# Kernel tuning notes

Hardware: AMD Instinct MI355X
Metric: run time of the kernel (lower is better)

Reference implementation:

```python
import jax, jax.numpy as jnp
import numpy as np

NQ = 6          # num_qubits
BS = 3          # basis_size (Pauli x,y,z)
HID = 32        # LSTM hidden size
SNAPS = 16      # max_num_snapshots
BATCH = 1024
DIM = 2 ** NQ   # 64


def _pauli():
    sx = np.array([[0., 1.], [1., 0.]], dtype=np.complex64)
    sy = np.array([[0., -1j], [1j, 0.]], dtype=np.complex64)
    sz = np.array([[1., 0.], [0., -1.]], dtype=np.complex64)
    return np.stack([sx, sy, sz], axis=0)


def setup_inputs():
    key = jax.random.key(0)
    ks = jax.random.split(key, 12)
    snapshot = jax.random.uniform(ks[0], (BATCH, NQ), jnp.float32, -1.0, 1.0)
    basis_comp_vector = jax.nn.softmax(
        jax.random.normal(ks[1], (BATCH, NQ, BS), jnp.float32), axis=-1)
    # valid density matrices: rho = A A^dag / tr
    ar = jax.random.normal(ks[2], (BATCH, DIM, DIM), jnp.float32)
    ai = jax.random.normal(ks[3], (BATCH, DIM, DIM), jnp.float32)
    A = ar + 1j * ai
    rho_c = jnp.einsum('bij,bkj->bik', A, jnp.conj(A))
    tr = jnp.trace(rho_c, axis1=1, axis2=2)[:, None, None]
    rho_c = rho_c / tr
    rho = jnp.stack([jnp.real(rho_c), jnp.imag(rho_c)], axis=1).astype(jnp.float32)
    h0 = jax.random.normal(ks[4], (BATCH, HID), jnp.float32)
    c0 = jax.random.normal(ks[5], (BATCH, HID), jnp.float32)
    in_dim = NQ + NQ * BS
    W_ih = jax.random.normal(ks[6], (4 * HID, in_dim), jnp.float32) * 0.1
    W_hh = jax.random.normal(ks[7], (4 * HID, HID), jnp.float32) * 0.1
    b_ih = jax.random.normal(ks[8], (4 * HID,), jnp.float32) * 0.05
    b_hh = jax.random.normal(ks[9], (4 * HID,), jnp.float32) * 0.05
    Wp = jax.random.normal(ks[10], (NQ, HID, BS), jnp.float32) * 0.1
    bp = jax.random.normal(ks[11], (NQ, BS), jnp.float32) * 0.05
    pauli = _pauli()
    basis_r = jnp.asarray(np.real(pauli), jnp.float32)
    basis_i = jnp.asarray(np.imag(pauli), jnp.float32)
    return {"snapshot": snapshot, "basis_comp_vector": basis_comp_vector,
            "rho": rho, "h0": h0, "c0": c0,
            "W_ih": W_ih, "W_hh": W_hh, "b_ih": b_ih, "b_hh": b_hh,
            "Wp": Wp, "bp": bp, "basis_r": basis_r, "basis_i": basis_i}


def _apply(p, M, axis, b):
    # apply 2x2 batched operator M [b,2,2] on tensor axis `axis` of p [b]+(2,)*2NQ
    pm = jnp.moveaxis(p, axis, 1)
    shp = pm.shape
    out = jnp.einsum('bij,bjr->bir', M, pm.reshape(b, 2, -1)).reshape(shp)
    return jnp.moveaxis(out, 1, axis)


def _measure(rho_t, probs, basis, basis_c, b):
    # sequential single-qubit measurement on the collapsing mixed state
    pc = probs.astype(jnp.complex64)
    M = jnp.einsum('bqs,sij->bqij', pc, basis)    # prob-mixed basis ops
    Mc = jnp.einsum('bqs,sij->bqij', pc, basis_c)
    p = rho_t
    outs = []
    for q in range(NQ):
        p = _apply(p, M[:, q], 1 + q, b)          # row index of qubit q
        p = _apply(p, Mc[:, q], 1 + NQ + q, b)    # col index of qubit q
        tr = jnp.trace(p.reshape(b, DIM, DIM), axis1=1, axis2=2)
        outs.append(jnp.real(tr))                 # measurement value s
        p = p / tr.reshape((b,) + (1,) * (2 * NQ))  # renormalized post-state
    return jnp.stack(outs, axis=1)                 # [b, NQ]


def _forward(snapshot, basis_comp_vector, rho, h0, c0,
             W_ih, W_hh, b_ih, b_hh, Wp, bp, basis_r, basis_i):
    b = snapshot.shape[0]
    basis = (basis_r + 1j * basis_i).astype(jnp.complex64)
    basis_c = jnp.conj(basis)
    rho_t = (rho[:, 0] + 1j * rho[:, 1]).astype(jnp.complex64)
    rho_t = rho_t.reshape((b,) + (2,) * (2 * NQ))

    x = jnp.concatenate([snapshot, basis_comp_vector.reshape(b, -1)], axis=-1)
    feats = [x]
    h, c = h0, c0
    for _ in range(SNAPS - 1):
        # torch LSTMCell: gate order i, f, g, o
        g = x @ W_ih.T + b_ih + h @ W_hh.T + b_hh
        gi, gf, gg, go = jnp.split(g, 4, axis=-1)
        c = jax.nn.sigmoid(gf) * c + jax.nn.sigmoid(gi) * jnp.tanh(gg)
        h = jax.nn.sigmoid(go) * jnp.tanh(c)
        probs = jax.nn.softmax(jnp.einsum('bh,qhs->bqs', h, Wp) + bp, axis=-1)
        # torch.Tensor(snapshot_batch) detaches -> stop_gradient
        snaps = jax.lax.stop_gradient(_measure(rho_t, probs, basis, basis_c, b))
        x = jnp.concatenate([snaps, probs.reshape(b, -1)], axis=-1)
        feats.append(x)

    # classical-shadow reconstruction: kron_q (I + 3 s_q B_q)/2, averaged
    eye2 = jnp.eye(2, dtype=jnp.complex64)
    acc = jnp.zeros((b, DIM, DIM), jnp.complex64)
    last_bv = None
    for xw in feats:
        shadow = xw[:, :NQ]
        bv = xw[:, NQ:].reshape(b, NQ, BS)
        last_bv = bv
        Bq = jnp.einsum('bqs,sij->bqij', bv.astype(jnp.complex64), basis)
        rc = (eye2 + 3.0 * shadow[:, :, None, None].astype(jnp.complex64) * Bq) / 2.0
        k = rc[:, 0]
        dd = 2
        for q in range(1, NQ):  # batched kron chain
            k = jnp.einsum('bij,bkl->bikjl', k, rc[:, q]).reshape(b, dd * 2, dd * 2)
            dd *= 2
        acc = acc + k
    rho_rec = acc / SNAPS
    out = jnp.stack([jnp.real(rho_rec), jnp.imag(rho_rec)], axis=1)
    return out, last_bv


def reference(snapshot, basis_comp_vector, rho, h0, c0,
              W_ih, W_hh, b_ih, b_hh, Wp, bp, basis_r, basis_i):
    return _forward(snapshot, basis_comp_vector, rho, h0, c0,
                    W_ih, W_hh, b_ih, b_hh, Wp, bp, basis_r, basis_i)
```

## Files before the change

kernel.cpp:

```cpp
#include <hip/hip_runtime.h>

#define NQ 6
#define HID 32
#define SNAPS 16
#define BATCH 1024
#define FSTRIDE 24
#define FTOT 384
#define KSTR 24
#define KF   192

typedef float vfloat4 __attribute__((ext_vector_type(4)));

__device__ __forceinline__ float sigm_f(float x) { return 1.0f / (1.0f + __expf(-x)); }
__device__ __forceinline__ float tanh_f(float x) { return 1.0f - 2.0f / (__expf(2.0f * x) + 1.0f); }

__device__ __forceinline__ float rl(float v, int l) {
    return __builtin_bit_cast(float, __builtin_amdgcn_readlane(__builtin_bit_cast(int, v), l));
}

__device__ __forceinline__ void rc_entry(float g, float b0, float b1, float b2,
                                         int i, int j, float& re, float& im) {
    if (i == j) { re = 0.5f + (i ? -g * b2 : g * b2); im = 0.0f; }
    else        { re = g * b0;  im = (i ? g * b1 : -g * b1); }
}

__global__ __launch_bounds__(64)
void lstm_kernel(const float* __restrict__ snapshot,
                 const float* __restrict__ bcv,
                 const float* __restrict__ h0,
                 const float* __restrict__ c0,
                 const float* __restrict__ W_ih,
                 const float* __restrict__ W_hh,
                 const float* __restrict__ b_ih,
                 const float* __restrict__ b_hh,
                 const float* __restrict__ Wp,
                 const float* __restrict__ bp,
                 float* __restrict__ feat_scratch,
                 float* __restrict__ out_tail)
{
    __shared__ __align__(16) float feat[FTOT];

    const int b = blockIdx.x;
    const int t = threadIdx.x;

    float4 wih0[6], wih1[6], whh0[8], whh1[8];
    {
        const float4* p0 = (const float4*)(W_ih + t * 24);
        const float4* p1 = (const float4*)(W_ih + (t + 64) * 24);
        #pragma unroll
        for (int k = 0; k < 6; ++k) { wih0[k] = p0[k]; wih1[k] = p1[k]; }
        const float4* q0 = (const float4*)(W_hh + t * 32);
        const float4* q1 = (const float4*)(W_hh + (t + 64) * 32);
        #pragma unroll
        for (int k = 0; k < 8; ++k) { whh0[k] = q0[k]; whh1[k] = q1[k]; }
    }
    const float bias0 = b_ih[t] + b_hh[t];
    const float bias1 = b_ih[t + 64] + b_hh[t + 64];

    float wp[32];
    float bpv = 0.0f, cst = 0.0f;
    if (t < 18) {
        int q = t / 3, s = t - 3 * q;
        #pragma unroll
        for (int k = 0; k < 32; ++k) wp[k] = Wp[q * 96 + 3 * k + s];
        bpv = bp[t];
    } else {
        #pragma unroll
        for (int k = 0; k < 32; ++k) wp[k] = 0.0f;
    }
    if (t < 32) cst = c0[b * 32 + t];

    float hval = (t < 32) ? h0[b * 32 + t] : 0.0f;
    float shh[32], sx[24];
    #pragma unroll
    for (int k = 0; k < 32; ++k) shh[k] = rl(hval, k);

    float x0v = 0.0f;
    if (t < 24) x0v = (t < 6) ? snapshot[b * 6 + t] : bcv[b * 18 + (t - 6)];
    if (t < 24) feat[t] = x0v;
    #pragma unroll
    for (int k = 0; k < 24; ++k) sx[k] = rl(x0v, k);

    for (int step = 0; step < SNAPS - 1; ++step) {
        float a0 = bias0, a1 = 0.0f, a2 = bias1, a3 = 0.0f;
        #pragma unroll
        for (int k = 0; k < 6; ++k) {
            a0 += sx[4 * k]     * wih0[k].x + sx[4 * k + 1] * wih0[k].y;
            a1 += sx[4 * k + 2] * wih0[k].z + sx[4 * k + 3] * wih0[k].w;
            a2 += sx[4 * k]     * wih1[k].x + sx[4 * k + 1] * wih1[k].y;
            a3 += sx[4 * k + 2] * wih1[k].z + sx[4 * k + 3] * wih1[k].w;
        }
        float a4 = 0.0f, a5 = 0.0f, a6 = 0.0f, a7 = 0.0f;
        #pragma unroll
        for (int k = 0; k < 8; ++k) {
            a4 += shh[4 * k]     * whh0[k].x + shh[4 * k + 1] * whh0[k].y;
            a5 += shh[4 * k + 2] * whh0[k].z + shh[4 * k + 3] * whh0[k].w;
            a6 += shh[4 * k]     * whh1[k].x + shh[4 * k + 1] * whh1[k].y;
            a7 += shh[4 * k + 2] * whh1[k].z + shh[4 * k + 3] * whh1[k].w;
        }
        float g0 = (a0 + a1) + (a4 + a5);
        float g1 = (a2 + a3) + (a6 + a7);

        float gf = __shfl(g0, (t + 32) & 63);
        float go = __shfl(g1, (t + 32) & 63);
        float gi = g0, gg = g1;

        cst = sigm_f(gf) * cst + sigm_f(gi) * tanh_f(gg);
        hval = sigm_f(go) * tanh_f(cst);

        #pragma unroll
        for (int k = 0; k < 32; ++k) shh[k] = rl(hval, k);

        float lg0 = bpv, lg1 = 0.0f;
        #pragma unroll
        for (int k = 0; k < 16; ++k) lg0 += shh[k] * wp[k];
        #pragma unroll
        for (int k = 16; k < 32; ++k) lg1 += shh[k] * wp[k];
        float logit = lg0 + lg1;

        int q3 = 3 * (t < 6 ? t : 0);
        float l0 = __shfl(logit, q3), l1 = __shfl(logit, q3 + 1), l2 = __shfl(logit, q3 + 2);
        float m = fmaxf(l0, fmaxf(l1, l2));
        float e0 = __expf(l0 - m), e1 = __expf(l1 - m), e2 = __expf(l2 - m);
        float inv = 1.0f / (e0 + e1 + e2);
        float p0 = e0 * inv, p1 = e1 * inv, p2 = e2 * inv;
        float snap = p0 * p0 + p1 * p1 + p2 * p2;

        if (t < 6) {
            float* fd = feat + (step + 1) * FSTRIDE;
            fd[t] = snap;
            fd[6 + 3 * t]     = p0;
            fd[6 + 3 * t + 1] = p1;
            fd[6 + 3 * t + 2] = p2;
        }

        #pragma unroll
        for (int q = 0; q < 6; ++q) {
            sx[q]          = rl(snap, q);
            sx[6 + 3 * q]     = rl(p0, q);
            sx[6 + 3 * q + 1] = rl(p1, q);
            sx[6 + 3 * q + 2] = rl(p2, q);
        }
    }

    __builtin_amdgcn_wave_barrier();
    float4* dst = (float4*)(feat_scratch + (size_t)b * 8192);
    const float4* srcf = (const float4*)feat;
    dst[t] = srcf[t];
    if (t < 32) dst[64 + t] = srcf[64 + t];
    if (t < 18) out_tail[b * 18 + t] = feat[15 * FSTRIDE + 6 + t];
}

__global__ __launch_bounds__(256, 4)
void recon_kernel(const float* feat_src,
                  float* out)
{
    __shared__ __align__(16) float sKA[16 * KF];
    __shared__ __align__(16) float sKB[16 * KF];
    __shared__ __align__(16) float feat[FTOT];

    const int b = blockIdx.x;
    const int t = threadIdx.x;

    if (t < 96)
        ((float4*)feat)[t] = ((const float4*)(feat_src + (size_t)b * 8192))[t];
    __syncthreads();

    for (int n = t; n < 2048; n += 256) {
        int f = n >> 7, r = n & 127;
        int half = r >> 6, a = r & 63;
        const float* fx = &feat[f * FSTRIDE];
        int i0 = (a >> 5) & 1, i1 = (a >> 4) & 1, i2 = (a >> 3) & 1;
        int j0 = (a >> 2) & 1, j1 = (a >> 1) & 1, j2 = a & 1;
        int q = 3 * half;
        float g0 = 1.5f * fx[q], g1 = 1.5f * fx[q + 1], g2 = 1.5f * fx[q + 2];
        const float* bb = fx + 6 + 3 * q;
        float r0, m0, r1, m1, r2, m2;
        rc_entry(g0, bb[0], bb[1], bb[2], i0, j0, r0, m0);
        rc_entry(g1, bb[3], bb[4], bb[5], i1, j1, r1, m1);
        rc_entry(g2, bb[6], bb[7], bb[8], i2, j2, r2, m2);
        float pr = r0 * r1 - m0 * m1, pi = r0 * m1 + m0 * r1;
        float qr = pr * r2 - pi * m2, qi = pr * m2 + pi * r2;
        int row = a >> 3, col = a & 7;
        if (half == 0) {
            int off = f * KF + col * KSTR + ((row & 1) ? (7 + row) : row);
            sKA[off] = qr; sKA[off + 1] = qi;
        } else {
            int off = f * KF + row * KSTR + 2 * col;
            sKB[off] = qr; sKB[off + 1] = qi;
        }
    }
    __syncthreads();

    const int u = t & 15, v = t >> 4;
    const float* baseA = sKA + (u >> 1) * KSTR + 8 * (v >> 3);
    const float* baseB = sKB + (v & 7) * KSTR + 8 * (u & 1);
    float accr[4][4], acci[4][4];
    #pragma unroll
    for (int e = 0; e < 4; ++e)
        #pragma unroll
        for (int d = 0; d < 4; ++d) { accr[e][d] = 0.0f; acci[e][d] = 0.0f; }

    #pragma unroll 2
    for (int f = 0; f < SNAPS; ++f) {
        float4 A0 = *(const float4*)(baseA + f * KF);
        float4 A1 = *(const float4*)(baseA + f * KF + 4);
        float4 B0 = *(const float4*)(baseB + f * KF);
        float4 B1 = *(const float4*)(baseB + f * KF + 4);
        float ar[4] = {A0.x, A0.z, A1.x, A1.z};
        float ai[4] = {A0.y, A0.w, A1.y, A1.w};
        float br[4] = {B0.x, B0.z, B1.x, B1.z};
        float bi[4] = {B0.y, B0.w, B1.y, B1.w};
        #pragma unroll
        for (int e = 0; e < 4; ++e)
            #pragma unroll
            for (int d = 0; d < 4; ++d) {
                accr[e][d] += ar[e] * br[d] - ai[e] * bi[d];
                acci[e][d] += ar[e] * bi[d] + ai[e] * br[d];
            }
    }

    const float s = 1.0f / 16.0f;
    float* outb = out + (size_t)b * 8192;
    #pragma unroll
    for (int e = 0; e < 4; ++e) {
        int i = v + 16 * e;
        vfloat4 r4 = { accr[e][0] * s, accr[e][1] * s, accr[e][2] * s, accr[e][3] * s };
        vfloat4 i4 = { acci[e][0] * s, acci[e][1] * s, acci[e][2] * s, acci[e][3] * s };
        __builtin_nontemporal_store(r4, (vfloat4*)(outb + i * 64 + 4 * u));
        __builtin_nontemporal_store(i4, (vfloat4*)(outb + 4096 + i * 64 + 4 * u));
    }
}

extern "C" void kernel_launch(void* const* d_in, const int* in_sizes, int n_in,
                              void* d_out, int out_size, void* d_ws, size_t ws_size,
                              hipStream_t stream) {
    const float* snapshot = (const float*)d_in[0];
    const float* bcv      = (const float*)d_in[1];
    const float* h0       = (const float*)d_in[3];
    const float* c0       = (const float*)d_in[4];
    const float* W_ih     = (const float*)d_in[5];
    const float* W_hh     = (const float*)d_in[6];
    const float* b_ih     = (const float*)d_in[7];
    const float* b_hh     = (const float*)d_in[8];
    const float* Wp       = (const float*)d_in[9];
    const float* bp       = (const float*)d_in[10];
    float* out = (float*)d_out;

    lstm_kernel<<<BATCH, 64, 0, stream>>>(
        snapshot, bcv, h0, c0, W_ih, W_hh, b_ih, b_hh, Wp, bp,
        out , out + (size_t)BATCH * 8192 );
    recon_kernel<<<BATCH, 256, 0, stream>>>(out, out);
}
```

Measured before the change: 133.2 us.

## Fuse LSTM and shadow reconstruction into one kernel with 128 threads

Merges the LSTM feature kernel and the reconstruction kernel into a single launch. One wave runs the recurrence and writes features to shared memory, then all 128 threads build the Kronecker factors and accumulate. This removes the global scratch round trip and the second launch. Each thread now computes two 4x4 complex tiles, doubling its register accumulators. The cost is that the second wave sits idle during the serial LSTM phase, and larger per-thread register use may lower occupancy.

```diff
diff --git a/kernel.cpp b/kernel.cpp
--- a/kernel.cpp
+++ b/kernel.cpp
@@ -24,136 +24,19 @@
     else        { re = g * b0;  im = (i ? g * b1 : -g * b1); }
 }
 
-__global__ __launch_bounds__(64)
-void lstm_kernel(const float* __restrict__ snapshot,
-                 const float* __restrict__ bcv,
-                 const float* __restrict__ h0,
-                 const float* __restrict__ c0,
-                 const float* __restrict__ W_ih,
-                 const float* __restrict__ W_hh,
-                 const float* __restrict__ b_ih,
-                 const float* __restrict__ b_hh,
-                 const float* __restrict__ Wp,
-                 const float* __restrict__ bp,
-                 float* __restrict__ feat_scratch,
-                 float* __restrict__ out_tail)
-{
-    __shared__ __align__(16) float feat[FTOT];
-
-    const int b = blockIdx.x;
-    const int t = threadIdx.x;
-
-    float4 wih0[6], wih1[6], whh0[8], whh1[8];
-    {
-        const float4* p0 = (const float4*)(W_ih + t * 24);
-        const float4* p1 = (const float4*)(W_ih + (t + 64) * 24);
-        #pragma unroll
-        for (int k = 0; k < 6; ++k) { wih0[k] = p0[k]; wih1[k] = p1[k]; }
-        const float4* q0 = (const float4*)(W_hh + t * 32);
-        const float4* q1 = (const float4*)(W_hh + (t + 64) * 32);
-        #pragma unroll
-        for (int k = 0; k < 8; ++k) { whh0[k] = q0[k]; whh1[k] = q1[k]; }
-    }
-    const float bias0 = b_ih[t] + b_hh[t];
-    const float bias1 = b_ih[t + 64] + b_hh[t + 64];
-
-    float wp[32];
-    float bpv = 0.0f, cst = 0.0f;
-    if (t < 18) {
-        int q = t / 3, s = t - 3 * q;
-        #pragma unroll
-        for (int k = 0; k < 32; ++k) wp[k] = Wp[q * 96 + 3 * k + s];
-        bpv = bp[t];
-    } else {
-        #pragma unroll
-        for (int k = 0; k < 32; ++k) wp[k] = 0.0f;
-    }
-    if (t < 32) cst = c0[b * 32 + t];
-
-    float hval = (t < 32) ? h0[b * 32 + t] : 0.0f;
-    float shh[32], sx[24];
-    #pragma unroll
-    for (int k = 0; k < 32; ++k) shh[k] = rl(hval, k);
-
-    float x0v = 0.0f;
-    if (t < 24) x0v = (t < 6) ? snapshot[b * 6 + t] : bcv[b * 18 + (t - 6)];
-    if (t < 24) feat[t] = x0v;
-    #pragma unroll
-    for (int k = 0; k < 24; ++k) sx[k] = rl(x0v, k);
-
-    for (int step = 0; step < SNAPS - 1; ++step) {
-        float a0 = bias0, a1 = 0.0f, a2 = bias1, a3 = 0.0f;
-        #pragma unroll
-        for (int k = 0; k < 6; ++k) {
-            a0 += sx[4 * k]     * wih0[k].x + sx[4 * k + 1] * wih0[k].y;
-            a1 += sx[4 * k + 2] * wih0[k].z + sx[4 * k + 3] * wih0[k].w;
-            a2 += sx[4 * k]     * wih1[k].x + sx[4 * k + 1] * wih1[k].y;
-            a3 += sx[4 * k + 2] * wih1[k].z + sx[4 * k + 3] * wih1[k].w;
-        }
-        float a4 = 0.0f, a5 = 0.0f, a6 = 0.0f, a7 = 0.0f;
-        #pragma unroll
-        for (int k = 0; k < 8; ++k) {
-            a4 += shh[4 * k]     * whh0[k].x + shh[4 * k + 1] * whh0[k].y;
-            a5 += shh[4 * k + 2] * whh0[k].z + shh[4 * k + 3] * whh0[k].w;
-            a6 += shh[4 * k]     * whh1[k].x + shh[4 * k + 1] * whh1[k].y;
-            a7 += shh[4 * k + 2] * whh1[k].z + shh[4 * k + 3] * whh1[k].w;
-        }
-        float g0 = (a0 + a1) + (a4 + a5);
-        float g1 = (a2 + a3) + (a6 + a7);
-
-        float gf = __shfl(g0, (t + 32) & 63);
-        float go = __shfl(g1, (t + 32) & 63);
-        float gi = g0, gg = g1;
-
-        cst = sigm_f(gf) * cst + sigm_f(gi) * tanh_f(gg);
-        hval = sigm_f(go) * tanh_f(cst);
-
-        #pragma unroll
-        for (int k = 0; k < 32; ++k) shh[k] = rl(hval, k);
-
-        float lg0 = bpv, lg1 = 0.0f;
-        #pragma unroll
-        for (int k = 0; k < 16; ++k) lg0 += shh[k] * wp[k];
-        #pragma unroll
-        for (int k = 16; k < 32; ++k) lg1 += shh[k] * wp[k];
-        float logit = lg0 + lg1;
-
-        int q3 = 3 * (t < 6 ? t : 0);
-        float l0 = __shfl(logit, q3), l1 = __shfl(logit, q3 + 1), l2 = __shfl(logit, q3 + 2);
-        float m = fmaxf(l0, fmaxf(l1, l2));
-        float e0 = __expf(l0 - m), e1 = __expf(l1 - m), e2 = __expf(l2 - m);
-        float inv = 1.0f / (e0 + e1 + e2);
-        float p0 = e0 * inv, p1 = e1 * inv, p2 = e2 * inv;
-        float snap = p0 * p0 + p1 * p1 + p2 * p2;
-
-        if (t < 6) {
-            float* fd = feat + (step + 1) * FSTRIDE;
-            fd[t] = snap;
-            fd[6 + 3 * t]     = p0;
-            fd[6 + 3 * t + 1] = p1;
-            fd[6 + 3 * t + 2] = p2;
-        }
-
-        #pragma unroll
-        for (int q = 0; q < 6; ++q) {
-            sx[q]          = rl(snap, q);
-            sx[6 + 3 * q]     = rl(p0, q);
-            sx[6 + 3 * q + 1] = rl(p1, q);
-            sx[6 + 3 * q + 2] = rl(p2, q);
-        }
-    }
-
-    __builtin_amdgcn_wave_barrier();
-    float4* dst = (float4*)(feat_scratch + (size_t)b * 8192);
-    const float4* srcf = (const float4*)feat;
-    dst[t] = srcf[t];
-    if (t < 32) dst[64 + t] = srcf[64 + t];
-    if (t < 18) out_tail[b * 18 + t] = feat[15 * FSTRIDE + 6 + t];
-}
-
-__global__ __launch_bounds__(256, 4)
-void recon_kernel(const float* feat_src,
-                  float* out)
+__global__ __launch_bounds__(128)
+void fused_kernel(const float* __restrict__ snapshot,
+                  const float* __restrict__ bcv,
+                  const float* __restrict__ h0,
+                  const float* __restrict__ c0,
+                  const float* __restrict__ W_ih,
+                  const float* __restrict__ W_hh,
+                  const float* __restrict__ b_ih,
+                  const float* __restrict__ b_hh,
+                  const float* __restrict__ Wp,
+                  const float* __restrict__ bp,
+                  float* __restrict__ out,
+                  float* __restrict__ out_tail)
 {
     __shared__ __align__(16) float sKA[16 * KF];
     __shared__ __align__(16) float sKB[16 * KF];
@@ -162,11 +45,112 @@
     const int b = blockIdx.x;
     const int t = threadIdx.x;
 
-    if (t < 96)
-        ((float4*)feat)[t] = ((const float4*)(feat_src + (size_t)b * 8192))[t];
+    if (t < 64) {
+        float4 wih0[6], wih1[6], whh0[8], whh1[8];
+        {
+            const float4* p0 = (const float4*)(W_ih + t * 24);
+            const float4* p1 = (const float4*)(W_ih + (t + 64) * 24);
+            #pragma unroll
+            for (int k = 0; k < 6; ++k) { wih0[k] = p0[k]; wih1[k] = p1[k]; }
+            const float4* q0 = (const float4*)(W_hh + t * 32);
+            const float4* q1 = (const float4*)(W_hh + (t + 64) * 32);
+            #pragma unroll
+            for (int k = 0; k < 8; ++k) { whh0[k] = q0[k]; whh1[k] = q1[k]; }
+        }
+        const float bias0 = b_ih[t] + b_hh[t];
+        const float bias1 = b_ih[t + 64] + b_hh[t + 64];
+
+        float wp[32];
+        float bpv = 0.0f, cst = 0.0f;
+        if (t < 18) {
+            int q = t / 3, s = t - 3 * q;
+            #pragma unroll
+            for (int k = 0; k < 32; ++k) wp[k] = Wp[q * 96 + 3 * k + s];
+            bpv = bp[t];
+        } else {
+            #pragma unroll
+            for (int k = 0; k < 32; ++k) wp[k] = 0.0f;
+        }
+        if (t < 32) cst = c0[b * 32 + t];
+
+        float hval = (t < 32) ? h0[b * 32 + t] : 0.0f;
+        float shh[32], sx[24];
+        #pragma unroll
+        for (int k = 0; k < 32; ++k) shh[k] = rl(hval, k);
+
+        float x0v = 0.0f;
+        if (t < 24) x0v = (t < 6) ? snapshot[b * 6 + t] : bcv[b * 18 + (t - 6)];
+        if (t < 24) feat[t] = x0v;
+        #pragma unroll
+        for (int k = 0; k < 24; ++k) sx[k] = rl(x0v, k);
+
+        for (int step = 0; step < SNAPS - 1; ++step) {
+            float a0 = bias0, a1 = 0.0f, a2 = bias1, a3 = 0.0f;
+            #pragma unroll
+            for (int k = 0; k < 6; ++k) {
+                a0 += sx[4 * k]     * wih0[k].x + sx[4 * k + 1] * wih0[k].y;
+                a1 += sx[4 * k + 2] * wih0[k].z + sx[4 * k + 3] * wih0[k].w;
+                a2 += sx[4 * k]     * wih1[k].x + sx[4 * k + 1] * wih1[k].y;
+                a3 += sx[4 * k + 2] * wih1[k].z + sx[4 * k + 3] * wih1[k].w;
+            }
+            float a4 = 0.0f, a5 = 0.0f, a6 = 0.0f, a7 = 0.0f;
+            #pragma unroll
+            for (int k = 0; k < 8; ++k) {
+                a4 += shh[4 * k]     * whh0[k].x + shh[4 * k + 1] * whh0[k].y;
+                a5 += shh[4 * k + 2] * whh0[k].z + shh[4 * k + 3] * whh0[k].w;
+                a6 += shh[4 * k]     * whh1[k].x + shh[4 * k + 1] * whh1[k].y;
+                a7 += shh[4 * k + 2] * whh1[k].z + shh[4 * k + 3] * whh1[k].w;
+            }
+            float g0 = (a0 + a1) + (a4 + a5);
+            float g1 = (a2 + a3) + (a6 + a7);
+
+            float gf = __shfl(g0, (t + 32) & 63);
+            float go = __shfl(g1, (t + 32) & 63);
+            float gi = g0, gg = g1;
+
+            cst = sigm_f(gf) * cst + sigm_f(gi) * tanh_f(gg);
+            hval = sigm_f(go) * tanh_f(cst);
+
+            #pragma unroll
+            for (int k = 0; k < 32; ++k) shh[k] = rl(hval, k);
+
+            float lg0 = bpv, lg1 = 0.0f;
+            #pragma unroll
+            for (int k = 0; k < 16; ++k) lg0 += shh[k] * wp[k];
+            #pragma unroll
+            for (int k = 16; k < 32; ++k) lg1 += shh[k] * wp[k];
+            float logit = lg0 + lg1;
+
+            int q3 = 3 * (t < 6 ? t : 0);
+            float l0 = __shfl(logit, q3), l1 = __shfl(logit, q3 + 1), l2 = __shfl(logit, q3 + 2);
+            float m = fmaxf(l0, fmaxf(l1, l2));
+            float e0 = __expf(l0 - m), e1 = __expf(l1 - m), e2 = __expf(l2 - m);
+            float inv = 1.0f / (e0 + e1 + e2);
+            float p0 = e0 * inv, p1 = e1 * inv, p2 = e2 * inv;
+            float snap = p0 * p0 + p1 * p1 + p2 * p2;
+
+            if (t < 6) {
+                float* fd = feat + (step + 1) * FSTRIDE;
+                fd[t] = snap;
+                fd[6 + 3 * t]     = p0;
+                fd[6 + 3 * t + 1] = p1;
+                fd[6 + 3 * t + 2] = p2;
+            }
+
+            #pragma unroll
+            for (int q = 0; q < 6; ++q) {
+                sx[q]             = rl(snap, q);
+                sx[6 + 3 * q]     = rl(p0, q);
+                sx[6 + 3 * q + 1] = rl(p1, q);
+                sx[6 + 3 * q + 2] = rl(p2, q);
+            }
+        }
+    }
     __syncthreads();
 
-    for (int n = t; n < 2048; n += 256) {
+    if (t >= 64 && t < 64 + 18) out_tail[b * 18 + (t - 64)] = feat[15 * FSTRIDE + 6 + (t - 64)];
+
+    for (int n = t; n < 2048; n += 128) {
         int f = n >> 7, r = n & 127;
         int half = r >> 6, a = r & 63;
         const float* fx = &feat[f * FSTRIDE];
@@ -192,44 +176,54 @@
     }
     __syncthreads();
 
-    const int u = t & 15, v = t >> 4;
-    const float* baseA = sKA + (u >> 1) * KSTR + 8 * (v >> 3);
-    const float* baseB = sKB + (v & 7) * KSTR + 8 * (u & 1);
-    float accr[4][4], acci[4][4];
+    const int u = t & 15, v0 = t >> 4;
+    const float* baseA = sKA + (u >> 1) * KSTR;
+    const float* baseB = sKB + v0 * KSTR + 8 * (u & 1);
+    float accr[2][4][4], acci[2][4][4];
     #pragma unroll
-    for (int e = 0; e < 4; ++e)
-        #pragma unroll
-        for (int d = 0; d < 4; ++d) { accr[e][d] = 0.0f; acci[e][d] = 0.0f; }
+    for (int h = 0; h < 2; ++h)
+        #pragma unroll
+        for (int e = 0; e < 4; ++e)
+            #pragma unroll
+            for (int d = 0; d < 4; ++d) { accr[h][e][d] = 0.0f; acci[h][e][d] = 0.0f; }
 
     #pragma unroll 2
     for (int f = 0; f < SNAPS; ++f) {
         float4 A0 = *(const float4*)(baseA + f * KF);
         float4 A1 = *(const float4*)(baseA + f * KF + 4);
+        float4 A2 = *(const float4*)(baseA + f * KF + 8);
+        float4 A3 = *(const float4*)(baseA + f * KF + 12);
         float4 B0 = *(const float4*)(baseB + f * KF);
         float4 B1 = *(const float4*)(baseB + f * KF + 4);
-        float ar[4] = {A0.x, A0.z, A1.x, A1.z};
-        float ai[4] = {A0.y, A0.w, A1.y, A1.w};
-        float br[4] = {B0.x, B0.z, B1.x, B1.z};
-        float bi[4] = {B0.y, B0.w, B1.y, B1.w};
+        float ar0[4] = {A0.x, A0.z, A1.x, A1.z};
+        float ai0[4] = {A0.y, A0.w, A1.y, A1.w};
+        float ar1[4] = {A2.x, A2.z, A3.x, A3.z};
+        float ai1[4] = {A2.y, A2.w, A3.y, A3.w};
+        float br[4]  = {B0.x, B0.z, B1.x, B1.z};
+        float bi[4]  = {B0.y, B0.w, B1.y, B1.w};
         #pragma unroll
         for (int e = 0; e < 4; ++e)
             #pragma unroll
             for (int d = 0; d < 4; ++d) {
-                accr[e][d] += ar[e] * br[d] - ai[e] * bi[d];
-                acci[e][d] += ar[e] * bi[d] + ai[e] * br[d];
+                accr[0][e][d] += ar0[e] * br[d] - ai0[e] * bi[d];
+                acci[0][e][d] += ar0[e] * bi[d] + ai0[e] * br[d];
+                accr[1][e][d] += ar1[e] * br[d] - ai1[e] * bi[d];
+                acci[1][e][d] += ar1[e] * bi[d] + ai1[e] * br[d];
             }
     }
 
     const float s = 1.0f / 16.0f;
     float* outb = out + (size_t)b * 8192;
     #pragma unroll
-    for (int e = 0; e < 4; ++e) {
-        int i = v + 16 * e;
-        vfloat4 r4 = { accr[e][0] * s, accr[e][1] * s, accr[e][2] * s, accr[e][3] * s };
-        vfloat4 i4 = { acci[e][0] * s, acci[e][1] * s, acci[e][2] * s, acci[e][3] * s };
-        __builtin_nontemporal_store(r4, (vfloat4*)(outb + i * 64 + 4 * u));
-        __builtin_nontemporal_store(i4, (vfloat4*)(outb + 4096 + i * 64 + 4 * u));
-    }
+    for (int h = 0; h < 2; ++h)
+        #pragma unroll
+        for (int e = 0; e < 4; ++e) {
+            int i = v0 + 8 * h + 16 * e;
+            vfloat4 r4 = { accr[h][e][0] * s, accr[h][e][1] * s, accr[h][e][2] * s, accr[h][e][3] * s };
+            vfloat4 i4 = { acci[h][e][0] * s, acci[h][e][1] * s, acci[h][e][2] * s, acci[h][e][3] * s };
+            __builtin_nontemporal_store(r4, (vfloat4*)(outb + i * 64 + 4 * u));
+            __builtin_nontemporal_store(i4, (vfloat4*)(outb + 4096 + i * 64 + 4 * u));
+        }
 }
 
 extern "C" void kernel_launch(void* const* d_in, const int* in_sizes, int n_in,
@@ -247,8 +241,7 @@
     const float* bp       = (const float*)d_in[10];
     float* out = (float*)d_out;
 
-    lstm_kernel<<<BATCH, 64, 0, stream>>>(
+    fused_kernel<<<BATCH, 128, 0, stream>>>(
         snapshot, bcv, h0, c0, W_ih, W_hh, b_ih, b_hh, Wp, bp,
-        out , out + (size_t)BATCH * 8192 );
-    recon_kernel<<<BATCH, 256, 0, stream>>>(out, out);
-}
+        out, out + (size_t)BATCH * 8192);
+}
```

After: 131.6 us. About the same (-1.2%).
